# Kernel tuning notes

Measured on AMD Instinct MI355X. Metric: run time of the kernel, lower is better.

Reference implementation:

```python
import jax, jax.numpy as jnp
import numpy as np

N_HEADS = 12
N_GROUPS = 32
EPS = 1e-5


def setup_inputs() -> dict:
    key = jax.random.key(0)
    ks = jax.random.split(key, 6)
    B, C, H, W = 8, 768, 32, 32
    EC, S = 768, 256
    x = jax.random.normal(ks[0], (B, C, H, W), dtype=jnp.float32)
    encoder_out = jax.random.normal(ks[1], (B, EC, S), dtype=jnp.float32)
    gn_w = jnp.ones((C,), jnp.float32)
    gn_b = jnp.zeros((C,), jnp.float32)
    qkv_w = jax.random.normal(ks[2], (3 * C, C), dtype=jnp.float32) * 0.02
    qkv_b = jnp.zeros((3 * C,), jnp.float32)
    enc_w = jax.random.normal(ks[3], (2 * C, EC), dtype=jnp.float32) * 0.02
    enc_b = jnp.zeros((2 * C,), jnp.float32)
    proj_w = jax.random.normal(ks[4], (C, C), dtype=jnp.float32) * 0.02
    proj_b = jnp.zeros((C,), jnp.float32)
    return {"x": x, "encoder_out": encoder_out, "gn_w": gn_w, "gn_b": gn_b,
            "qkv_w": qkv_w, "qkv_b": qkv_b, "enc_w": enc_w, "enc_b": enc_b,
            "proj_w": proj_w, "proj_b": proj_b}


def _group_norm(x, w, b):
    # x: [B, C, T]
    B, C, T = x.shape
    xg = x.reshape(B, N_GROUPS, C // N_GROUPS, T)
    mean = jnp.mean(xg, axis=(2, 3), keepdims=True)
    var = jnp.var(xg, axis=(2, 3), keepdims=True)
    xn = ((xg - mean) * jax.lax.rsqrt(var + EPS)).reshape(B, C, T)
    return xn * w[None, :, None] + b[None, :, None]


def reference(x, encoder_out, gn_w, gn_b, qkv_w, qkv_b, enc_w, enc_b, proj_w, proj_b):
    B, C, Hs, Ws = x.shape
    T = Hs * Ws
    ch = C // N_HEADS
    xf = x.reshape(B, C, T)
    xn = _group_norm(xf, gn_w, gn_b)
    # 1x1 conv == channel matmul
    qkv = jnp.einsum('oc,bct->bot', qkv_w, xn) + qkv_b[None, :, None]  # [B, 3C, T]
    # torch layout: per-head contiguous blocks of [q, k, v]
    qkv = qkv.reshape(B * N_HEADS, 3 * ch, T)
    q, k, v = qkv[:, :ch], qkv[:, ch:2 * ch], qkv[:, 2 * ch:]
    ekv = jnp.einsum('oc,bcs->bos', enc_w, encoder_out) + enc_b[None, :, None]  # [B, 2C, S]
    ekv = ekv.reshape(B * N_HEADS, 2 * ch, -1)
    ek, ev = ekv[:, :ch], ekv[:, ch:]
    k = jnp.concatenate([ek, k], axis=-1)  # [BH, ch, S+T]
    v = jnp.concatenate([ev, v], axis=-1)
    scale = 1.0 / np.sqrt(np.sqrt(ch))
    w = jnp.einsum('bct,bcs->bts', q * scale, k * scale)  # [BH, T, S+T]
    w = jax.nn.softmax(w.astype(jnp.float32), axis=-1).astype(q.dtype)
    a = jnp.einsum('bts,bcs->bct', w, v).reshape(B, C, T)
    h = jnp.einsum('oc,bct->bot', proj_w, a) + proj_b[None, :, None]
    return (xf + h).reshape(B, C, Hs, Ws)
```

## Files before the change

kernel.cpp:

```cpp
#include <hip/hip_runtime.h>

typedef __attribute__((ext_vector_type(8))) short bf16x8;
typedef __attribute__((ext_vector_type(4))) float f32x4;
typedef __attribute__((ext_vector_type(16))) float f32x16;
typedef __attribute__((ext_vector_type(4))) float float4v;
typedef __attribute__((ext_vector_type(4))) unsigned short ushort4v;
typedef __attribute__((ext_vector_type(8))) unsigned short ushort8v;

#define DEVINL __device__ __forceinline__


DEVINL unsigned short f2bf(float f) {
  union { float f; unsigned u; } v; v.f = f;
  unsigned r = (v.u + 0x7fffu + ((v.u >> 16) & 1u)) >> 16;
  return (unsigned short)r;
}
DEVINL float bf2f(unsigned short h) {
  union { unsigned u; float f; } v; v.u = ((unsigned)h) << 16;
  return v.f;
}
DEVINL float exp2a(float x) {
  float r; asm("v_exp_f32 %0, %1" : "=v"(r) : "v"(x)); return r;
}
DEVINL unsigned cvtpk(float lo, float hi) {
  unsigned r;
  asm("v_cvt_pk_bf16_f32 %0, %1, %2" : "=v"(r) : "v"(lo), "v"(hi));
  return r;
}
DEVINL void gload16(const void* g, void* l) {
  __builtin_amdgcn_global_load_lds(
      (const __attribute__((address_space(1))) unsigned*)g,
      (__attribute__((address_space(3))) unsigned*)l, 16, 0, 0);
}
DEVINL void plswap(unsigned& a, unsigned& b) {
  asm("v_permlane32_swap_b32 %0, %1" : "+v"(a), "+v"(b));
}
DEVINL bf16x8 mkfrag(unsigned a, unsigned b, unsigned c, unsigned d) {
  union { unsigned u[4]; bf16x8 v; } x;
  x.u[0] = a; x.u[1] = b; x.u[2] = c; x.u[3] = d;
  return x.v;
}
#define WAITV0 asm volatile("s_waitcnt vmcnt(0)" ::: "memory")
#define WAITV3 asm volatile("s_waitcnt vmcnt(3)" ::: "memory")
#define WAITV4 asm volatile("s_waitcnt vmcnt(4)" ::: "memory")
#define RBAR  __builtin_amdgcn_s_barrier()

__global__ __launch_bounds__(256) void k_prep(const float* __restrict__ s0,
                                              const float* __restrict__ s1,
                                              const float* __restrict__ s2,
                                              unsigned short* __restrict__ wd,
                                              const float* __restrict__ x,
                                              const float* __restrict__ gw,
                                              const float* __restrict__ gb,
                                              unsigned short* __restrict__ xnt,
                                              const float* __restrict__ enc,
                                              unsigned short* __restrict__ et) {
  __shared__ unsigned short L[64 * 72];
  __shared__ float rs[4], rss[4], stat[2];
  int blk = blockIdx.x, tid = threadIdx.x;

  if (blk < 3456) {
    int i = blk * 256 + tid;
    const float* s; int off;
    if (i < 442368)      { s = s0; off = i; }
    else if (i < 737280) { s = s1; off = i - 442368; }
    else                 { s = s2; off = i - 737280; }
    float4v v = *(const float4v*)(s + (size_t)off * 4);
    ushort4v o;
    o[0] = f2bf(v[0]); o[1] = f2bf(v[1]); o[2] = f2bf(v[2]); o[3] = f2bf(v[3]);
    *(ushort4v*)(wd + (size_t)i * 4) = o;
    return;
  }
  if (blk < 3712) {
    int e = blk - 3456, g = e & 31, b = e >> 5;
    const float* xb = x + ((size_t)b * 768 + g * 24) * 1024;
    float s = 0.f, ss = 0.f;
    for (int i = tid; i < 6144; i += 256) {
      float4v v = *(const float4v*)(xb + (size_t)i * 4);
      s += v[0] + v[1] + v[2] + v[3];
      ss += v[0] * v[0] + v[1] * v[1] + v[2] * v[2] + v[3] * v[3];
    }
    #pragma unroll
    for (int o = 32; o > 0; o >>= 1) { s += __shfl_down(s, o); ss += __shfl_down(ss, o); }
    int wv_ = tid >> 6;
    if ((tid & 63) == 0) { rs[wv_] = s; rss[wv_] = ss; }
    __syncthreads();
    if (tid == 0) {
      float S = rs[0] + rs[1] + rs[2] + rs[3], SS = rss[0] + rss[1] + rss[2] + rss[3];
      float mean = S / 24576.f;
      float var = SS / 24576.f - mean * mean;
      stat[0] = mean; stat[1] = rsqrtf(fmaxf(var, 0.f) + 1e-5f);
    }
    __syncthreads();
    float mean = stat[0], rstd = stat[1];
    float wv[24], bv[24];
    #pragma unroll
    for (int c = 0; c < 24; ++c) { wv[c] = gw[g * 24 + c]; bv[c] = gb[g * 24 + c]; }
    for (int it = 0; it < 4; ++it) {
      int t = it * 256 + tid;
      ushort8v ov[3];
      #pragma unroll
      for (int c = 0; c < 24; ++c) {
        float v = xb[(size_t)c * 1024 + t];
        ov[c >> 3][c & 7] = f2bf((v - mean) * rstd * wv[c] + bv[c]);
      }
      ushort8v* dst = (ushort8v*)(xnt + ((size_t)(b * 1024 + t)) * 768 + g * 24);
      dst[0] = ov[0]; dst[1] = ov[1]; dst[2] = ov[2];
    }
    return;
  }
  int e = blk - 3712;
  int ct = (e % 12) * 64, st = ((e / 12) & 3) * 64, b = e / 48;
  #pragma unroll
  for (int it = 0; it < 4; ++it) {
    int idx = it * 256 + tid; int r = idx >> 4, ch = idx & 15;
    float4v v = *(const float4v*)(enc + ((size_t)(b * 768 + ct + r)) * 256 + st + ch * 4);
    ushort4v o;
    o[0] = f2bf(v[0]); o[1] = f2bf(v[1]); o[2] = f2bf(v[2]); o[3] = f2bf(v[3]);
    *(ushort4v*)&L[r * 72 + ch * 4] = o;
  }
  __syncthreads();
  #pragma unroll
  for (int it = 0; it < 2; ++it) {
    int idx = it * 256 + tid; int s = idx >> 3, ch = idx & 7;
    ushort8v o;
    #pragma unroll
    for (int j = 0; j < 8; ++j) o[j] = L[(ch * 8 + j) * 72 + s];
    *(ushort8v*)(et + ((size_t)(b * 256 + st + s)) * 768 + ct + ch * 8) = o;
  }
}

__global__ __launch_bounds__(256) void k_vcat(const unsigned short* __restrict__ qkvt,
                                              const unsigned short* __restrict__ ekvt,
                                              unsigned short* __restrict__ vcat) {
  int s0 = blockIdx.x * 64, bh = blockIdx.y, b = bh / 12, h = bh % 12, tid = threadIdx.x;
  __shared__ unsigned short L[64 * 72];
  #pragma unroll
  for (int it = 0; it < 2; ++it) {
    int idx = it * 256 + tid; int s = idx >> 3, ch = idx & 7;
    int sg = s0 + s;
    const unsigned short* src = (sg < 256)
        ? ekvt + ((size_t)(b * 256 + sg)) * 1536 + h * 128 + 64 + ch * 8
        : qkvt + ((size_t)(b * 1024 + sg - 256)) * 2304 + h * 192 + 128 + ch * 8;
    *(ushort8v*)&L[s * 72 + ch * 8] = *(const ushort8v*)src;
  }
  __syncthreads();
  #pragma unroll
  for (int it = 0; it < 2; ++it) {
    int idx = it * 256 + tid; int c = idx >> 3, ch = idx & 7;
    ushort8v o;
    #pragma unroll
    for (int j = 0; j < 8; ++j) o[j] = L[(ch * 8 + j) * 72 + c];
    *(ushort8v*)(vcat + ((size_t)bh * 64 + c) * 1280 + s0 + ch * 8) = o;
  }
}

__global__ __launch_bounds__(256, 3) void k_g12(const unsigned short* __restrict__ A1,
                                                const unsigned short* __restrict__ B1,
                                                const float* __restrict__ bias1,
                                                unsigned short* __restrict__ out1,
                                                const unsigned short* __restrict__ A2,
                                                const unsigned short* __restrict__ B2,
                                                const float* __restrict__ bias2,
                                                unsigned short* __restrict__ out2) {
  const int K = 768;
  int gid = blockIdx.x;
  const unsigned short *A, *Bp; const float* bias; unsigned short* outp; int N, m0, n0;
  if (gid < 1152) {
    A = A1; Bp = B1; bias = bias1; outp = out1; N = 2304;
    m0 = (gid & 63) * 128; n0 = (gid >> 6) * 128;
  } else {
    int g = gid - 1152;
    A = A2; Bp = B2; bias = bias2; outp = out2; N = 1536;
    m0 = (g & 15) * 128; n0 = (g >> 4) * 128;
  }
  const unsigned short* Ab = A + (size_t)m0 * K;
  const unsigned short* Bb = Bp + (size_t)n0 * K;
  __shared__ unsigned short As[3][4096], Bs[3][4096];
  int tid = threadIdx.x, lane = tid & 63, w = tid >> 6;
  int l31 = lane & 31, hi2 = lane >> 5;
  int wm = (w >> 1) * 64, wn = (w & 1) * 64;
  int sr = tid >> 2, sc = tid & 3;
  int schunk = (sc ^ ((sr >> 1) & 3)) * 8;
  const unsigned short* gA = Ab + (size_t)sr * K + schunk;
  const unsigned short* gB = Bb + (size_t)sr * K + schunk;

  f32x16 acc[2][2];
  #pragma unroll
  for (int i = 0; i < 2; ++i)
    #pragma unroll
    for (int j = 0; j < 2; ++j)
      #pragma unroll
      for (int r = 0; r < 16; ++r) acc[i][j][r] = 0.f;

  auto stageAB = [&](int buf, int k0) {
    unsigned short* ad = &As[buf][0] + w * 512;
    unsigned short* bd = &Bs[buf][0] + w * 512;
    gload16(gA + k0, ad);
    gload16(gA + (size_t)64 * K + k0, ad + 2048);
    gload16(gB + k0, bd);
    gload16(gB + (size_t)64 * K + k0, bd + 2048);
  };
  auto comp = [&](int buf) {
    const char* abase = (const char*)&As[buf][0];
    const char* bbase = (const char*)&Bs[buf][0];
    #pragma unroll
    for (int kk = 0; kk < 2; ++kk) {
      bf16x8 afr[2], bfr[2];
      #pragma unroll
      for (int ri = 0; ri < 2; ++ri) {
        int row = wm + ri * 32 + l31;
        int sl = (kk * 2 + hi2) ^ ((row >> 1) & 3);
        afr[ri] = *(const bf16x8*)(abase + row * 64 + sl * 16);
      }
      #pragma unroll
      for (int ci = 0; ci < 2; ++ci) {
        int row = wn + ci * 32 + l31;
        int sl = (kk * 2 + hi2) ^ ((row >> 1) & 3);
        bfr[ci] = *(const bf16x8*)(bbase + row * 64 + sl * 16);
      }
      #pragma unroll
      for (int ri = 0; ri < 2; ++ri)
        #pragma unroll
        for (int ci = 0; ci < 2; ++ci)
          acc[ri][ci] = __builtin_amdgcn_mfma_f32_32x32x16_bf16(afr[ri], bfr[ci],
                                                                acc[ri][ci], 0, 0, 0);
    }
  };

  stageAB(0, 0);
  stageAB(1, 32);
  WAITV4;
  RBAR;
  int cur = 0;
  for (int kt = 0; kt < 22; ++kt) {
    int pre = cur - 1; if (pre < 0) pre += 3;
    stageAB(pre, (kt + 2) * 32);
    comp(cur);
    WAITV4;
    RBAR;
    ++cur; if (cur == 3) cur = 0;
  }
  comp(cur);
  WAITV0;
  RBAR;
  ++cur; if (cur == 3) cur = 0;
  comp(cur);

  #pragma unroll
  for (int ri = 0; ri < 2; ++ri) {
    #pragma unroll
    for (int ci = 0; ci < 2; ++ci) {
      #pragma unroll
      for (int rg = 0; rg < 16; ++rg) {
        int row = m0 + wm + ri * 32 + (rg & 3) + 8 * (rg >> 2) + 4 * hi2;
        int col = n0 + wn + ci * 32 + l31;
        outp[(size_t)row * N + col] = f2bf(acc[ri][ci][rg] + bias[col]);
      }
    }
  }
}

__global__ __launch_bounds__(256, 3) void k_gemm3(const unsigned short* __restrict__ A,
                                                  const unsigned short* __restrict__ B,
                                                  const float* __restrict__ bias,
                                                  const float* __restrict__ resid,
                                                  float* __restrict__ outp,
                                                  int N, int K,
                                                  long sB, long sO, long sR) {
  int bz = blockIdx.z;
  int m0 = blockIdx.x * 64, n0 = blockIdx.y * 128;
  const unsigned short* Ab = A + (size_t)m0 * K;
  const unsigned short* Bb = B + (size_t)bz * sB + (size_t)n0 * K;
  __shared__ unsigned short As[3][2048], Bs[3][4096];
  int tid = threadIdx.x, lane = tid & 63, w = tid >> 6;
  int l31 = lane & 31, hi2 = lane >> 5;
  int wm = (w >> 1) * 32, wn = (w & 1) * 64;
  int sr = tid >> 2, sc = tid & 3;
  int schunk = (sc ^ ((sr >> 1) & 3)) * 8;
  const unsigned short* gA = Ab + (size_t)sr * K + schunk;
  const unsigned short* gB = Bb + (size_t)sr * K + schunk;

  f32x16 acc[2];
  #pragma unroll
  for (int j = 0; j < 2; ++j)
    #pragma unroll
    for (int r = 0; r < 16; ++r) acc[j][r] = 0.f;

  auto stageAB = [&](int buf, int k0) {
    unsigned short* ad = &As[buf][0] + w * 512;
    unsigned short* bd = &Bs[buf][0] + w * 512;
    gload16(gA + k0, ad);
    gload16(gB + k0, bd);
    gload16(gB + (size_t)64 * K + k0, bd + 2048);
  };
  auto comp = [&](int buf) {
    const char* abase = (const char*)&As[buf][0];
    const char* bbase = (const char*)&Bs[buf][0];
    #pragma unroll
    for (int kk = 0; kk < 2; ++kk) {
      bf16x8 afr, bfr[2];
      {
        int row = wm + l31;
        int sl = (kk * 2 + hi2) ^ ((row >> 1) & 3);
        afr = *(const bf16x8*)(abase + row * 64 + sl * 16);
      }
      #pragma unroll
      for (int ci = 0; ci < 2; ++ci) {
        int row = wn + ci * 32 + l31;
        int sl = (kk * 2 + hi2) ^ ((row >> 1) & 3);
        bfr[ci] = *(const bf16x8*)(bbase + row * 64 + sl * 16);
      }
      #pragma unroll
      for (int ci = 0; ci < 2; ++ci)
        acc[ci] = __builtin_amdgcn_mfma_f32_32x32x16_bf16(afr, bfr[ci], acc[ci], 0, 0, 0);
    }
  };

  int nk = K >> 5;
  stageAB(0, 0);
  stageAB(1, 32);
  WAITV3;
  RBAR;
  int cur = 0;
  for (int kt = 0; kt < nk - 2; ++kt) {
    int pre = cur - 1; if (pre < 0) pre += 3;
    stageAB(pre, (kt + 2) * 32);
    comp(cur);
    WAITV3;
    RBAR;
    ++cur; if (cur == 3) cur = 0;
  }
  comp(cur);
  WAITV0;
  RBAR;
  ++cur; if (cur == 3) cur = 0;
  comp(cur);

  #pragma unroll
  for (int ci = 0; ci < 2; ++ci) {
    #pragma unroll
    for (int rg = 0; rg < 16; ++rg) {
      int row = m0 + wm + (rg & 3) + 8 * (rg >> 2) + 4 * hi2;
      int col = n0 + wn + ci * 32 + l31;
      float v = acc[ci][rg] + bias[row] + resid[(size_t)bz * sR + (size_t)row * N + col];
      outp[(size_t)bz * sO + (size_t)row * N + col] = v;
    }
  }
}

__global__ __launch_bounds__(256, 3) void k_attn(const unsigned short* __restrict__ qkvt,
                                                 const unsigned short* __restrict__ ekvt,
                                                 const unsigned short* __restrict__ vcat,
                                                 unsigned short* __restrict__ at) {
  int bid = blockIdx.x;
  int swb = (bid & 7) * 96 + (bid >> 3);
  int t0 = (swb & 7) * 128, bh = swb >> 3, b = bh / 12, h = bh % 12;
  int tid = threadIdx.x, w = tid >> 6, lane = tid & 63;
  int ql = lane & 31, hi = lane >> 5;
  __shared__ unsigned short Ks[2][4096], Vs[2][4096];

  const float QSC = 0.125f * 1.44269504089f;
  bf16x8 aq[4];
  const unsigned short* qrow = qkvt + ((size_t)(b * 1024 + t0 + w * 32 + ql)) * 2304 + h * 192;
  #pragma unroll
  for (int jc = 0; jc < 4; ++jc) {
    ushort8v qv = *(const ushort8v*)(qrow + jc * 16 + hi * 8);
    bf16x8 o;
    #pragma unroll
    for (int e = 0; e < 8; ++e) o[e] = (short)f2bf(bf2f(qv[e]) * QSC);
    aq[jc] = o;
  }

  int rloc = w * 16 + (lane >> 3);
  int chunk = (lane & 7) ^ (lane >> 3);
  const unsigned short* ke_st = ekvt + ((size_t)(b * 256 + rloc)) * 1536 + h * 128 + chunk * 8;
  const unsigned short* kq_st = qkvt + ((long)b * 1024 - 256 + rloc) * 2304 + h * 192 + 64 + chunk * 8;
  const unsigned short* v_st  = vcat + ((size_t)(bh * 64 + rloc)) * 1280 + chunk * 8;
  unsigned short* kd = &Ks[0][0] + w * 1024;
  unsigned short* vd = &Vs[0][0] + w * 1024;

  auto stage = [&](int nb, int tn) {
    const unsigned short* ks;
    size_t rstep;
    if (tn < 4) { ks = ke_st + (size_t)tn * 64 * 1536; rstep = 8 * 1536; }
    else        { ks = kq_st + (size_t)tn * 64 * 2304; rstep = 8 * 2304; }
    unsigned short* kdd = kd + nb * 4096;
    unsigned short* vdd = vd + nb * 4096;
    const unsigned short* vs = v_st + tn * 64;
    gload16(ks, kdd);
    gload16(ks + rstep, kdd + 512);
    gload16(vs, vdd);
    gload16(vs + 8 * 1280, vdd + 512);
  };

  stage(0, 0);
  WAITV0;
  __syncthreads();

  f32x16 acc0, acc1;
  #pragma unroll
  for (int r = 0; r < 16; ++r) { acc0[r] = 0.f; acc1[r] = 0.f; }
  float l = 0.f;
  int xp = (ql & 7) << 4;

  for (int t = 0; t < 20; ++t) {
    int cur = t & 1;
    if (t < 19) stage(cur ^ 1, t + 1);

    f32x16 sf0, sf1;
    #pragma unroll
    for (int r = 0; r < 16; ++r) { sf0[r] = 0.f; sf1[r] = 0.f; }
    const char* kbase = (const char*)&Ks[cur][0] + ql * 128;
    __builtin_amdgcn_s_setprio(1);
    #pragma unroll
    for (int jc = 0; jc < 4; ++jc) {
      int off = (jc * 32 + hi * 16) ^ xp;
      bf16x8 k0f = *(const bf16x8*)(kbase + off);
      bf16x8 k1f = *(const bf16x8*)(kbase + 4096 + off);
      sf0 = __builtin_amdgcn_mfma_f32_32x32x16_bf16(k0f, aq[jc], sf0, 0, 0, 0);
      sf1 = __builtin_amdgcn_mfma_f32_32x32x16_bf16(k1f, aq[jc], sf1, 0, 0, 0);
    }
    __builtin_amdgcn_s_setprio(0);

    float pe[32];
    #pragma unroll
    for (int i = 0; i < 16; ++i) pe[i] = exp2a(sf0[i]);
    #pragma unroll
    for (int i = 0; i < 16; ++i) pe[16 + i] = exp2a(sf1[i]);

    const char* vbase = (const char*)&Vs[cur][0] + ql * 128;
    #pragma unroll
    for (int sb = 0; sb < 2; ++sb) {
      unsigned pk[8];
      #pragma unroll
      for (int i = 0; i < 8; ++i)
        pk[i] = cvtpk(pe[sb * 16 + 2 * i], pe[sb * 16 + 2 * i + 1]);
      plswap(pk[0], pk[2]);
      plswap(pk[1], pk[3]);
      plswap(pk[4], pk[6]);
      plswap(pk[5], pk[7]);
      bf16x8 fj0 = mkfrag(pk[0], pk[1], pk[2], pk[3]);
      bf16x8 fj1 = mkfrag(pk[4], pk[5], pk[6], pk[7]);
      __builtin_amdgcn_s_setprio(1);
      #pragma unroll
      for (int jj = 0; jj < 2; ++jj) {
        int off = (sb * 64 + jj * 32 + hi * 16) ^ xp;
        bf16x8 v0f = *(const bf16x8*)(vbase + off);
        bf16x8 v1f = *(const bf16x8*)(vbase + 4096 + off);
        bf16x8 pf = jj ? fj1 : fj0;
        acc0 = __builtin_amdgcn_mfma_f32_32x32x16_bf16(v0f, pf, acc0, 0, 0, 0);
        acc1 = __builtin_amdgcn_mfma_f32_32x32x16_bf16(v1f, pf, acc1, 0, 0, 0);
      }
      __builtin_amdgcn_s_setprio(0);
    }

    float s0 = 0.f, s1 = 0.f, s2 = 0.f, s3 = 0.f;
    #pragma unroll
    for (int i = 0; i < 8; ++i) {
      s0 += pe[i]; s1 += pe[8 + i]; s2 += pe[16 + i]; s3 += pe[24 + i];
    }
    l += (s0 + s1) + (s2 + s3);

    if (t < 19) WAITV0;
    __syncthreads();
  }

  l += __shfl_xor(l, 32);
  float rl = 1.f / l;
  unsigned short* orow = at + ((size_t)(b * 1024 + t0 + w * 32 + ql)) * 768 + h * 64;
  #pragma unroll
  for (int cb = 0; cb < 2; ++cb) {
    #pragma unroll
    for (int g = 0; g < 4; ++g) {
      int c = cb * 32 + g * 8 + hi * 4;
      ushort4v o;
      #pragma unroll
      for (int i = 0; i < 4; ++i) {
        float v = (cb ? acc1[g * 4 + i] : acc0[g * 4 + i]) * rl;
        o[i] = f2bf(v);
      }
      *(ushort4v*)(orow + c) = o;
    }
  }
}

extern "C" void kernel_launch(void* const* d_in, const int* in_sizes, int n_in,
                              void* d_out, int out_size, void* d_ws, size_t ws_size,
                              hipStream_t stream) {
  const float* x      = (const float*)d_in[0];
  const float* enc    = (const float*)d_in[1];
  const float* gn_w   = (const float*)d_in[2];
  const float* gn_b   = (const float*)d_in[3];
  const float* qkv_w  = (const float*)d_in[4];
  const float* qkv_b  = (const float*)d_in[5];
  const float* enc_w  = (const float*)d_in[6];
  const float* enc_b  = (const float*)d_in[7];
  const float* proj_w = (const float*)d_in[8];
  const float* proj_b = (const float*)d_in[9];
  float* out = (float*)d_out;

  char* ws = (char*)d_ws;
  unsigned short* w_qkv = (unsigned short*)(ws + 0);
  unsigned short* w_enc = (unsigned short*)(ws + 3538944);
  unsigned short* w_prj = (unsigned short*)(ws + 5898240);
  unsigned short* xn_t  = (unsigned short*)(ws + 7077888);
  unsigned short* enc_t = (unsigned short*)(ws + 19660800);
  unsigned short* qkv_t = (unsigned short*)(ws + 22806528);
  unsigned short* ekv_t = (unsigned short*)(ws + 60555264);
  unsigned short* vcat  = (unsigned short*)(ws + 66846720);
  unsigned short* a_t   = xn_t;

  k_prep<<<4096, 256, 0, stream>>>(qkv_w, enc_w, proj_w, w_qkv,
                                   x, gn_w, gn_b, xn_t, enc, enc_t);
  k_g12<<<1344, 256, 0, stream>>>(xn_t, w_qkv, qkv_b, qkv_t,
                                  enc_t, w_enc, enc_b, ekv_t);
  k_vcat<<<dim3(20, 96), 256, 0, stream>>>(qkv_t, ekv_t, vcat);
  k_attn<<<dim3(768), 256, 0, stream>>>(qkv_t, ekv_t, vcat, a_t);
  k_gemm3<<<dim3(12, 8, 8), 256, 0, stream>>>(w_prj, a_t, proj_b, x, out,
                                              1024, 768, 786432L, 786432L, 786432L);
}
```

Before: 156.9 us.

## Split attention KV loop across two wave groups with LDS reduction

The attention kernel now launches 512 threads per block. Two halves of four waves each process half of the 20 key/value tiles for the same 128 queries, each with its own double-buffered LDS. The partial accumulators and row sums are then combined through shared memory before normalization and store. The aim is a shorter serial loop per wave and more parallelism per block. In exchange, LDS per block doubles, occupancy drops from 3 to 2 blocks, and a final exchange pass is added.

Measured after the change: 165.4 us. +5.4%, slower.

```diff
diff --git a/kernel.cpp b/kernel.cpp
--- a/kernel.cpp
+++ b/kernel.cpp
@@ -349,7 +349,7 @@
   }
 }
 
-__global__ __launch_bounds__(256, 3) void k_attn(const unsigned short* __restrict__ qkvt,
+__global__ __launch_bounds__(512, 2) void k_attn(const unsigned short* __restrict__ qkvt,
                                                  const unsigned short* __restrict__ ekvt,
                                                  const unsigned short* __restrict__ vcat,
                                                  unsigned short* __restrict__ at) {
@@ -357,12 +357,13 @@
   int swb = (bid & 7) * 96 + (bid >> 3);
   int t0 = (swb & 7) * 128, bh = swb >> 3, b = bh / 12, h = bh % 12;
   int tid = threadIdx.x, w = tid >> 6, lane = tid & 63;
+  int half = w >> 2, wq = w & 3;
   int ql = lane & 31, hi = lane >> 5;
-  __shared__ unsigned short Ks[2][4096], Vs[2][4096];
+  __shared__ unsigned short Ks[2][2][4096], Vs[2][2][4096];
 
   const float QSC = 0.125f * 1.44269504089f;
   bf16x8 aq[4];
-  const unsigned short* qrow = qkvt + ((size_t)(b * 1024 + t0 + w * 32 + ql)) * 2304 + h * 192;
+  const unsigned short* qrow = qkvt + ((size_t)(b * 1024 + t0 + wq * 32 + ql)) * 2304 + h * 192;
   #pragma unroll
   for (int jc = 0; jc < 4; ++jc) {
     ushort8v qv = *(const ushort8v*)(qrow + jc * 16 + hi * 8);
@@ -372,21 +373,19 @@
     aq[jc] = o;
   }
 
-  int rloc = w * 16 + (lane >> 3);
+  int rloc = wq * 16 + (lane >> 3);
   int chunk = (lane & 7) ^ (lane >> 3);
   const unsigned short* ke_st = ekvt + ((size_t)(b * 256 + rloc)) * 1536 + h * 128 + chunk * 8;
   const unsigned short* kq_st = qkvt + ((long)b * 1024 - 256 + rloc) * 2304 + h * 192 + 64 + chunk * 8;
   const unsigned short* v_st  = vcat + ((size_t)(bh * 64 + rloc)) * 1280 + chunk * 8;
-  unsigned short* kd = &Ks[0][0] + w * 1024;
-  unsigned short* vd = &Vs[0][0] + w * 1024;
 
   auto stage = [&](int nb, int tn) {
     const unsigned short* ks;
     size_t rstep;
     if (tn < 4) { ks = ke_st + (size_t)tn * 64 * 1536; rstep = 8 * 1536; }
     else        { ks = kq_st + (size_t)tn * 64 * 2304; rstep = 8 * 2304; }
-    unsigned short* kdd = kd + nb * 4096;
-    unsigned short* vdd = vd + nb * 4096;
+    unsigned short* kdd = &Ks[half][nb][wq * 1024];
+    unsigned short* vdd = &Vs[half][nb][wq * 1024];
     const unsigned short* vs = v_st + tn * 64;
     gload16(ks, kdd);
     gload16(ks + rstep, kdd + 512);
@@ -394,7 +393,7 @@
     gload16(vs + 8 * 1280, vdd + 512);
   };
 
-  stage(0, 0);
+  stage(0, half * 10);
   WAITV0;
   __syncthreads();
 
@@ -404,14 +403,15 @@
   float l = 0.f;
   int xp = (ql & 7) << 4;
 
-  for (int t = 0; t < 20; ++t) {
-    int cur = t & 1;
-    if (t < 19) stage(cur ^ 1, t + 1);
+  for (int tt = 0; tt < 10; ++tt) {
+    int t = half * 10 + tt;
+    int cur = tt & 1;
+    if (tt < 9) stage(cur ^ 1, t + 1);
 
     f32x16 sf0, sf1;
     #pragma unroll
     for (int r = 0; r < 16; ++r) { sf0[r] = 0.f; sf1[r] = 0.f; }
-    const char* kbase = (const char*)&Ks[cur][0] + ql * 128;
+    const char* kbase = (const char*)&Ks[half][cur][0] + ql * 128;
     __builtin_amdgcn_s_setprio(1);
     #pragma unroll
     for (int jc = 0; jc < 4; ++jc) {
@@ -429,7 +429,7 @@
     #pragma unroll
     for (int i = 0; i < 16; ++i) pe[16 + i] = exp2a(sf1[i]);
 
-    const char* vbase = (const char*)&Vs[cur][0] + ql * 128;
+    const char* vbase = (const char*)&Vs[half][cur][0] + ql * 128;
     #pragma unroll
     for (int sb = 0; sb < 2; ++sb) {
       unsigned pk[8];
@@ -462,25 +462,45 @@
     }
     l += (s0 + s1) + (s2 + s3);
 
-    if (t < 19) WAITV0;
+    if (tt < 9) WAITV0;
     __syncthreads();
   }
 
-  l += __shfl_xor(l, 32);
-  float rl = 1.f / l;
-  unsigned short* orow = at + ((size_t)(b * 1024 + t0 + w * 32 + ql)) * 768 + h * 64;
-  #pragma unroll
-  for (int cb = 0; cb < 2; ++cb) {
-    #pragma unroll
-    for (int g = 0; g < 4; ++g) {
-      int c = cb * 32 + g * 8 + hi * 4;
-      ushort4v o;
-      #pragma unroll
-      for (int i = 0; i < 4; ++i) {
-        float v = (cb ? acc1[g * 4 + i] : acc0[g * 4 + i]) * rl;
-        o[i] = f2bf(v);
-      }
-      *(ushort4v*)(orow + c) = o;
+  float* xch = (float*)&Ks[0][0][0];
+  float* xl  = (float*)&Vs[0][0][0];
+  int slot = wq * 64 + lane;
+  if (half == 1) {
+    #pragma unroll
+    for (int r = 0; r < 16; ++r) {
+      xch[r * 256 + slot] = acc0[r];
+      xch[(16 + r) * 256 + slot] = acc1[r];
+    }
+    xl[slot] = l;
+  }
+  __syncthreads();
+  if (half == 0) {
+    #pragma unroll
+    for (int r = 0; r < 16; ++r) {
+      acc0[r] += xch[r * 256 + slot];
+      acc1[r] += xch[(16 + r) * 256 + slot];
+    }
+    l += xl[slot];
+    l += __shfl_xor(l, 32);
+    float rl = 1.f / l;
+    unsigned short* orow = at + ((size_t)(b * 1024 + t0 + wq * 32 + ql)) * 768 + h * 64;
+    #pragma unroll
+    for (int cb = 0; cb < 2; ++cb) {
+      #pragma unroll
+      for (int g = 0; g < 4; ++g) {
+        int c = cb * 32 + g * 8 + hi * 4;
+        ushort4v o;
+        #pragma unroll
+        for (int i = 0; i < 4; ++i) {
+          float v = (cb ? acc1[g * 4 + i] : acc0[g * 4 + i]) * rl;
+          o[i] = f2bf(v);
+        }
+        *(ushort4v*)(orow + c) = o;
+      }
     }
   }
 }
@@ -516,7 +536,7 @@
   k_g12<<<1344, 256, 0, stream>>>(xn_t, w_qkv, qkv_b, qkv_t,
                                   enc_t, w_enc, enc_b, ekv_t);
   k_vcat<<<dim3(20, 96), 256, 0, stream>>>(qkv_t, ekv_t, vcat);
-  k_attn<<<dim3(768), 256, 0, stream>>>(qkv_t, ekv_t, vcat, a_t);
+  k_attn<<<dim3(768), 512, 0, stream>>>(qkv_t, ekv_t, vcat, a_t);
   k_gemm3<<<dim3(12, 8, 8), 256, 0, stream>>>(w_prj, a_t, proj_b, x, out,
                                               1024, 768, 786432L, 786432L, 786432L);
 }
```
